# Performance work log

Hardware: AMD Instinct MI355X
Metric: run time of the kernel (lower is better)

The kernel has to match this reference:

```python
import jax, jax.numpy as jnp
import numpy as np

N = 50000
IN_DIM = 128
HEADS = 4
HEAD_DIM = IN_DIM // HEADS
TYPE_NUM = 3
E = 800000
NEG_SLOPE = 0.2


def setup_inputs() -> dict:
    key = jax.random.key(0)
    k1, k2, k3, k4, k5 = jax.random.split(key, 5)
    embedding = jax.random.normal(k1, (N, IN_DIM), dtype=jnp.float32)
    edges = jax.random.randint(k2, (TYPE_NUM, 2, E), 0, N, dtype=jnp.int32)
    W = jax.random.normal(k3, (TYPE_NUM, IN_DIM, HEADS, HEAD_DIM), dtype=jnp.float32) * 0.05
    a_src = jax.random.normal(k4, (TYPE_NUM, HEADS, HEAD_DIM), dtype=jnp.float32) * 0.05
    a_dst = jax.random.normal(k5, (TYPE_NUM, HEADS, HEAD_DIM), dtype=jnp.float32) * 0.05
    return {"embedding": embedding, "edges": edges, "W": W, "a_src": a_src, "a_dst": a_dst}


def _gat_layer(x, ei, W_t, asrc_t, adst_t):
    # x: [N, IN_DIM]; ei: [2, E]; W_t: [IN_DIM, H, D]
    h = jnp.einsum('nd,dhk->nhk', x, W_t)                  # [N, H, D]
    e_src = jnp.sum(h * asrc_t, axis=-1)                   # [N, H]
    e_dst = jnp.sum(h * adst_t, axis=-1)                   # [N, H]
    src, dst = ei[0], ei[1]
    e = jax.nn.leaky_relu(e_src[src] + e_dst[dst], NEG_SLOPE)  # [E, H]
    m = jax.ops.segment_max(e, dst, num_segments=N)        # [N, H]
    e = jnp.exp(e - m[dst])
    denom = jax.ops.segment_sum(e, dst, num_segments=N)    # [N, H]
    msg = h[src] * e[:, :, None]                           # [E, H, D]
    agg = jax.ops.segment_sum(msg, dst, num_segments=N)    # [N, H, D]
    out = agg / (denom[:, :, None] + 1e-9)
    return jax.nn.elu(out.reshape(N, HEADS * HEAD_DIM))


def reference(embedding, edges, W, a_src, a_dst):
    features_gat = [_gat_layer(embedding, edges[i], W[i], a_src[i], a_dst[i])
                    for i in range(TYPE_NUM)]
    # NOTE: the original module (faithfully) also uses the GAT layers for the
    # 'gcn' branch: features_gcn = [self.gat_layers[i](...) for ...]
    features_gcn = [_gat_layer(embedding, edges[i], W[i], a_src[i], a_dst[i])
                    for i in range(TYPE_NUM)]
    return (jnp.stack(features_gat), jnp.stack(features_gcn))
```

## Files before the change

kernel.cpp:

```cpp
#include <hip/hip_runtime.h>
#include <hip/hip_fp16.h>
#include <math.h>

#define NN 50000
#define IND 128
#define NH 4
#define NE 800000
#define NT 3
#define NSLOPE 0.2f

#define TILE 64
#define NBPT 782
#define NBTOT (NT * NBPT)
#define BCAP 1280

#define SCB ((NT * NE + 8191) / 8192)
#define GXB ((NN + 127) / 128)

typedef _Float16 f16x8 __attribute__((ext_vector_type(8)));
typedef float    f32x4 __attribute__((ext_vector_type(4)));

__global__ __launch_bounds__(256) void prep_kernel(
    const float* __restrict__ W, __half* __restrict__ wt16g, int* __restrict__ gcursor)
{
    int idx = blockIdx.x * 256 + threadIdx.x;
    if (idx < NT * IND * IND) {
        int t = idx / (IND * IND), r = idx - t * (IND * IND);
        int k = r >> 7, c = r & 127;
        wt16g[((size_t)t * IND + c) * IND + k] = (__half)W[idx];
    }
    if (idx < NBTOT) gcursor[idx] = idx * BCAP;
}

__global__ __launch_bounds__(512) void scatter_gemm_kernel(
    const int* __restrict__ edges, int* __restrict__ gcursor, unsigned* __restrict__ bucketed,
    const float* __restrict__ x, const __half* __restrict__ wt16g,
    const float* __restrict__ asrc, const float* __restrict__ adst,
    __half* __restrict__ h16, float* __restrict__ es, float* __restrict__ ed)
{
    __shared__ __align__(16) char ldsbuf[34816];
    const int tid = threadIdx.x;

    if (blockIdx.x < SCB) {
        int* cnt = (int*)ldsbuf;
        int* bas = cnt + NBTOT;
        for (int i = tid; i < NBTOT; i += 512) cnt[i] = 0;
        __syncthreads();
        const long long gtot = (long long)NT * NE;
        const long long g0 = (long long)blockIdx.x * 8192;
        long long g1 = g0 + 8192; if (g1 > gtot) g1 = gtot;
        for (long long g = g0 + tid; g < g1; g += 512) {
            int t = (g >= 2LL * NE) ? 2 : (g >= NE ? 1 : 0);
            int e = (int)(g - (long long)t * NE);
            int d = edges[(size_t)t * 2 * NE + NE + e];
            atomicAdd(&cnt[t * NBPT + (d >> 6)], 1);
        }
        __syncthreads();
        for (int i = tid; i < NBTOT; i += 512) {
            int c = cnt[i];
            bas[i] = c ? atomicAdd(&gcursor[i], c) : 0;
            cnt[i] = 0;
        }
        __syncthreads();
        for (long long g = g0 + tid; g < g1; g += 512) {
            int t = (g >= 2LL * NE) ? 2 : (g >= NE ? 1 : 0);
            int e = (int)(g - (long long)t * NE);
            const int* eb = edges + (size_t)t * 2 * NE;
            int s = eb[e], d = eb[NE + e];
            int bg = t * NBPT + (d >> 6);
            int pos = bas[bg] + atomicAdd(&cnt[bg], 1);
            bucketed[pos] = (unsigned)s | ((unsigned)(d & 63) << 16);
        }
        return;
    }

    const int bx = blockIdx.x - SCB;
    const int t  = bx / GXB;
    const int gx = bx - t * GXB;
    __half* tile = (__half*)ldsbuf;
    const int wid = tid >> 6, lane = tid & 63;
    __half* tl = tile + wid * (16 * 136);
    const int l15 = lane & 15, l4 = lane >> 4;
    const int r0 = gx * 128 + wid * 16;
    const bool active = (r0 < NN);

    const __half* wt = wt16g + (size_t)t * IND * IND;
    const float* xrow = x + (size_t)((active ? r0 : 0) + l15) * IND;

    f32x4 acc[8];
    #pragma unroll
    for (int i = 0; i < 8; i++) acc[i] = (f32x4){0.f, 0.f, 0.f, 0.f};

    #pragma unroll
    for (int ks = 0; ks < 4; ks++) {
        const int kb = ks * 32 + l4 * 8;
        float4 x0 = *reinterpret_cast<const float4*>(xrow + kb);
        float4 x1 = *reinterpret_cast<const float4*>(xrow + kb + 4);
        f16x8 af;
        af[0] = (_Float16)x0.x; af[1] = (_Float16)x0.y;
        af[2] = (_Float16)x0.z; af[3] = (_Float16)x0.w;
        af[4] = (_Float16)x1.x; af[5] = (_Float16)x1.y;
        af[6] = (_Float16)x1.z; af[7] = (_Float16)x1.w;
        #pragma unroll
        for (int ct = 0; ct < 8; ct++) {
            f16x8 bf = *reinterpret_cast<const f16x8*>(wt + (size_t)(ct * 16 + l15) * IND + kb);
            acc[ct] = __builtin_amdgcn_mfma_f32_16x16x32_f16(af, bf, acc[ct], 0, 0, 0);
        }
    }

    #pragma unroll
    for (int ct = 0; ct < 8; ct++)
        #pragma unroll
        for (int r = 0; r < 4; r++)
            tl[(l4 * 4 + r) * 136 + ct * 16 + l15] = (__half)acc[ct][r];
    __syncthreads();

    if (active) {
        #pragma unroll
        for (int i = 0; i < 4; i++) {
            int c = lane + 64 * i;
            int row = c >> 4, off = (c & 15) * 8;
            f16x8 v = *reinterpret_cast<const f16x8*>(tl + row * 136 + off);
            *reinterpret_cast<f16x8*>(h16 + ((size_t)t * NN + r0 + row) * IND + off) = v;
        }
        int row16 = lane >> 2, head = lane & 3;
        const __half* hr = tl + row16 * 136 + head * 32;
        const float* av = asrc + ((size_t)t * NH + head) * 32;
        const float* bv = adst + ((size_t)t * NH + head) * 32;
        float se = 0.f, de = 0.f;
        #pragma unroll
        for (int jj = 0; jj < 4; jj++) {
            f16x8 hv = *reinterpret_cast<const f16x8*>(hr + jj * 8);
            #pragma unroll
            for (int j = 0; j < 8; j++) {
                float hf = (float)hv[j];
                se = fmaf(hf, av[jj * 8 + j], se);
                de = fmaf(hf, bv[jj * 8 + j], de);
            }
        }
        int n = r0 + row16;
        es[((size_t)t * NN + n) * NH + head] = se;
        ed[((size_t)t * NN + n) * NH + head] = de;
    }
}

__global__ __launch_bounds__(512) void gat_bucket_kernel(
    const unsigned* __restrict__ bucketed, const int* __restrict__ gcursor,
    const float* __restrict__ es, const float* __restrict__ ed,
    const __half* __restrict__ h16, float* __restrict__ out)
{
    __shared__ unsigned pk[BCAP];
    __shared__ unsigned srt[BCAP];
    __shared__ int hist[TILE], scn[TILE], cur[TILE];
    const int bg = blockIdx.x;
    const int t = bg / NBPT;
    const int node0 = (bg - t * NBPT) * TILE;
    const int tid = threadIdx.x;
    const int base = bg * BCAP;
    const int cnt = gcursor[bg] - base;

    if (tid < TILE) { hist[tid] = 0; cur[tid] = 0; }
    __syncthreads();
    for (int i = tid; i < cnt; i += 512) {
        unsigned v = bucketed[base + i];
        pk[i] = v;
        atomicAdd(&hist[(v >> 16) & 63u], 1);
    }
    __syncthreads();
    if (tid < 64) {
        int v = hist[tid];
        int inc = v;
        #pragma unroll
        for (int off = 1; off < 64; off <<= 1) {
            int n = __shfl_up(inc, off, 64);
            if (tid >= off) inc += n;
        }
        scn[tid] = inc - v;
    }
    __syncthreads();
    for (int i = tid; i < cnt; i += 512) {
        unsigned v = pk[i];
        int dl = (int)((v >> 16) & 63u);
        int pos = scn[dl] + atomicAdd(&cur[dl], 1);
        srt[pos] = v & 0xFFFFu;
    }
    __syncthreads();

    const int wid = tid >> 6, lane = tid & 63;
    const int el = lane >> 5, dl2 = lane & 31;
    const int hsel = dl2 >> 3;
    const float* es_t = es + (size_t)t * NN * NH;
    const __half* h16_t = h16 + (size_t)t * NN * IND;

    for (int j = 0; j < 8; j++) {
        const int dloc = wid * 8 + j;
        const int node = node0 + dloc;
        if (node >= NN) break;
        const int beg = scn[dloc], nE = hist[dloc];
        const float edv = ed[((size_t)t * NN + node) * NH + (lane & 3)];

        float a0 = 0.f, a1 = 0.f, a2 = 0.f, a3 = 0.f, dsum = 0.f;

        for (int b2 = 0; b2 < nE; b2 += 16) {
            int ne = nE - b2; if (ne > 16) ne = 16;
            const int ei = lane >> 2;
            float wv = 0.f; int sv = 0;
            if (ei < ne) {
                sv = (int)srt[beg + b2 + ei];
                float s = es_t[(sv << 2) + (lane & 3)] + edv;
                s = s > 0.f ? s : NSLOPE * s;
                wv = __expf(s);
                dsum += wv;
            }
            int kk = 0;
            for (; kk + 2 <= ne; kk += 2) {
                int k2 = kk + el;
                int   sb = __shfl(sv, k2 << 2, 64);
                float wb = __shfl(wv, (k2 << 2) | hsel, 64);
                uint2 hv = *reinterpret_cast<const uint2*>(h16_t + ((size_t)sb << 7) + (dl2 << 2));
                asm("v_fma_mix_f32 %0, %1, %2, %0 op_sel:[0,0,0] op_sel_hi:[1,0,0]" : "+v"(a0) : "v"(hv.x), "v"(wb));
                asm("v_fma_mix_f32 %0, %1, %2, %0 op_sel:[1,0,0] op_sel_hi:[1,0,0]" : "+v"(a1) : "v"(hv.x), "v"(wb));
                asm("v_fma_mix_f32 %0, %1, %2, %0 op_sel:[0,0,0] op_sel_hi:[1,0,0]" : "+v"(a2) : "v"(hv.y), "v"(wb));
                asm("v_fma_mix_f32 %0, %1, %2, %0 op_sel:[1,0,0] op_sel_hi:[1,0,0]" : "+v"(a3) : "v"(hv.y), "v"(wb));
            }
            if (kk < ne) {
                int   sb = __shfl(sv, kk << 2, 64);
                float wb = __shfl(wv, (kk << 2) | hsel, 64);
                if (el == 0) {
                    uint2 hv = *reinterpret_cast<const uint2*>(h16_t + ((size_t)sb << 7) + (dl2 << 2));
                    asm("v_fma_mix_f32 %0, %1, %2, %0 op_sel:[0,0,0] op_sel_hi:[1,0,0]" : "+v"(a0) : "v"(hv.x), "v"(wb));
                    asm("v_fma_mix_f32 %0, %1, %2, %0 op_sel:[1,0,0] op_sel_hi:[1,0,0]" : "+v"(a1) : "v"(hv.x), "v"(wb));
                    asm("v_fma_mix_f32 %0, %1, %2, %0 op_sel:[0,0,0] op_sel_hi:[1,0,0]" : "+v"(a2) : "v"(hv.y), "v"(wb));
                    asm("v_fma_mix_f32 %0, %1, %2, %0 op_sel:[1,0,0] op_sel_hi:[1,0,0]" : "+v"(a3) : "v"(hv.y), "v"(wb));
                }
            }
        }

        #pragma unroll
        for (int m = 4; m <= 32; m <<= 1) dsum += __shfl_xor(dsum, m, 64);
        a0 += __shfl_xor(a0, 32, 64);
        a1 += __shfl_xor(a1, 32, 64);
        a2 += __shfl_xor(a2, 32, 64);
        a3 += __shfl_xor(a3, 32, 64);
        float dn = __shfl(dsum, hsel, 64) + 1e-9f;

        if (el == 0) {
            float v0 = a0 / dn, v1 = a1 / dn, v2 = a2 / dn, v3 = a3 / dn;
            f32x4 o;
            o[0] = v0 > 0.f ? v0 : expm1f(v0);
            o[1] = v1 > 0.f ? v1 : expm1f(v1);
            o[2] = v2 > 0.f ? v2 : expm1f(v2);
            o[3] = v3 > 0.f ? v3 : expm1f(v3);
            float* obase = out + (size_t)t * NN * IND + ((size_t)node << 7) + (dl2 << 2);
            __builtin_nontemporal_store(o, reinterpret_cast<f32x4*>(obase));
            __builtin_nontemporal_store(o, reinterpret_cast<f32x4*>(obase + (size_t)NT * NN * IND));
        }
    }
}

extern "C" void kernel_launch(void* const* d_in, const int* in_sizes, int n_in,
                              void* d_out, int out_size, void* d_ws, size_t ws_size,
                              hipStream_t stream)
{
    const float* x     = (const float*)d_in[0];
    const int*   edges = (const int*)d_in[1];
    const float* W     = (const float*)d_in[2];
    const float* asrc  = (const float*)d_in[3];
    const float* adst  = (const float*)d_in[4];
    float* out = (float*)d_out;

    char* p = (char*)d_ws;
    __half*   h16      = (__half*)p;   p += (size_t)NT * NN * IND * 2;
    float*    es       = (float*)p;    p += (size_t)NT * NN * NH * 4;
    float*    ed       = (float*)p;    p += (size_t)NT * NN * NH * 4;
    int*      gcursor  = (int*)p;      p += (size_t)NBTOT * 4;
    __half*   wt16g    = (__half*)p;   p += (size_t)NT * IND * IND * 2;
    unsigned* bucketed = (unsigned*)p; p += ((size_t)NBTOT * BCAP + 1024) * 4;

    prep_kernel<<<(NT * IND * IND + 255) / 256, 256, 0, stream>>>(W, wt16g, gcursor);
    scatter_gemm_kernel<<<SCB + NT * GXB, 512, 0, stream>>>(
        edges, gcursor, bucketed, x, wt16g, asrc, adst, h16, es, ed);
    gat_bucket_kernel<<<NBTOT, 512, 0, stream>>>(bucketed, gcursor, es, ed, h16, out);
}
```

Before: 226.5 us.

## Aggregate raw features before projection and fold attention vectors into W

Uses linearity to swap projection and aggregation. Per-head attention logits are computed straight from x through precomputed W·a vectors with a small MFMA. Edges then gather a shared fp16 copy of x instead of per-type projected h. The per-head aggregated features (512 wide per node) then go through a per-type MFMA GEMM with fused ELU and a dual store. This shrinks the gather working set to one fp16 copy of x shared across types, at the cost of 4x-wider gather accumulators, a g16 round trip, and six extra serialized launches.

```diff
diff --git a/kernel.cpp b/kernel.cpp
--- a/kernel.cpp
+++ b/kernel.cpp
@@ -15,13 +15,14 @@
 #define BCAP 1280
 
 #define SCB ((NT * NE + 8191) / 8192)
-#define GXB ((NN + 127) / 128)
+#define CVB ((NN + 127) / 128)
 
 typedef _Float16 f16x8 __attribute__((ext_vector_type(8)));
 typedef float    f32x4 __attribute__((ext_vector_type(4)));
 
 __global__ __launch_bounds__(256) void prep_kernel(
-    const float* __restrict__ W, __half* __restrict__ wt16g, int* __restrict__ gcursor)
+    const float* __restrict__ W, const float* __restrict__ asrc, const float* __restrict__ adst,
+    __half* __restrict__ wt16g, __half* __restrict__ vab16, int* __restrict__ gcursor)
 {
     int idx = blockIdx.x * 256 + threadIdx.x;
     if (idx < NT * IND * IND) {
@@ -29,21 +30,32 @@
         int k = r >> 7, c = r & 127;
         wt16g[((size_t)t * IND + c) * IND + k] = (__half)W[idx];
     }
+    if (idx < 32 * 128) {
+        int c = idx >> 7, d = idx & 127;
+        float acc = 0.f;
+        if (c < 24) {
+            int cc = c < 12 ? c : c - 12;
+            int t = cc >> 2, hd = cc & 3;
+            const float* wrow = W + ((size_t)(t * IND + d) * NH + hd) * 32;
+            const float* av = (c < 12 ? asrc : adst) + ((size_t)t * NH + hd) * 32;
+            #pragma unroll
+            for (int dk = 0; dk < 32; dk++) acc = fmaf(wrow[dk], av[dk], acc);
+        }
+        vab16[idx] = (__half)acc;
+    }
     if (idx < NBTOT) gcursor[idx] = idx * BCAP;
 }
 
-__global__ __launch_bounds__(512) void scatter_gemm_kernel(
+__global__ __launch_bounds__(512) void scatter_conv_kernel(
     const int* __restrict__ edges, int* __restrict__ gcursor, unsigned* __restrict__ bucketed,
-    const float* __restrict__ x, const __half* __restrict__ wt16g,
-    const float* __restrict__ asrc, const float* __restrict__ adst,
-    __half* __restrict__ h16, float* __restrict__ es, float* __restrict__ ed)
-{
-    __shared__ __align__(16) char ldsbuf[34816];
+    const float* __restrict__ x, const __half* __restrict__ vab16,
+    __half* __restrict__ x16, float* __restrict__ es, float* __restrict__ ed)
+{
     const int tid = threadIdx.x;
 
     if (blockIdx.x < SCB) {
-        int* cnt = (int*)ldsbuf;
-        int* bas = cnt + NBTOT;
+        __shared__ int cnt[NBTOT];
+        __shared__ int bas[NBTOT];
         for (int i = tid; i < NBTOT; i += 512) cnt[i] = 0;
         __syncthreads();
         const long long gtot = (long long)NT * NE;
@@ -75,86 +87,58 @@
     }
 
     const int bx = blockIdx.x - SCB;
-    const int t  = bx / GXB;
-    const int gx = bx - t * GXB;
-    __half* tile = (__half*)ldsbuf;
     const int wid = tid >> 6, lane = tid & 63;
-    __half* tl = tile + wid * (16 * 136);
     const int l15 = lane & 15, l4 = lane >> 4;
-    const int r0 = gx * 128 + wid * 16;
-    const bool active = (r0 < NN);
-
-    const __half* wt = wt16g + (size_t)t * IND * IND;
-    const float* xrow = x + (size_t)((active ? r0 : 0) + l15) * IND;
-
-    f32x4 acc[8];
-    #pragma unroll
-    for (int i = 0; i < 8; i++) acc[i] = (f32x4){0.f, 0.f, 0.f, 0.f};
-
+    const int r0 = bx * 128 + wid * 16;
+    if (r0 >= NN) return;
+
+    const float* xrow = x + (size_t)(r0 + l15) * IND;
+    __half* x16row = x16 + (size_t)(r0 + l15) * IND;
+
+    f32x4 acc0 = {0.f,0.f,0.f,0.f}, acc1 = {0.f,0.f,0.f,0.f};
     #pragma unroll
     for (int ks = 0; ks < 4; ks++) {
         const int kb = ks * 32 + l4 * 8;
-        float4 x0 = *reinterpret_cast<const float4*>(xrow + kb);
-        float4 x1 = *reinterpret_cast<const float4*>(xrow + kb + 4);
+        float4 a = *reinterpret_cast<const float4*>(xrow + kb);
+        float4 b = *reinterpret_cast<const float4*>(xrow + kb + 4);
         f16x8 af;
-        af[0] = (_Float16)x0.x; af[1] = (_Float16)x0.y;
-        af[2] = (_Float16)x0.z; af[3] = (_Float16)x0.w;
-        af[4] = (_Float16)x1.x; af[5] = (_Float16)x1.y;
-        af[6] = (_Float16)x1.z; af[7] = (_Float16)x1.w;
-        #pragma unroll
-        for (int ct = 0; ct < 8; ct++) {
-            f16x8 bf = *reinterpret_cast<const f16x8*>(wt + (size_t)(ct * 16 + l15) * IND + kb);
-            acc[ct] = __builtin_amdgcn_mfma_f32_16x16x32_f16(af, bf, acc[ct], 0, 0, 0);
-        }
-    }
-
-    #pragma unroll
-    for (int ct = 0; ct < 8; ct++)
-        #pragma unroll
-        for (int r = 0; r < 4; r++)
-            tl[(l4 * 4 + r) * 136 + ct * 16 + l15] = (__half)acc[ct][r];
-    __syncthreads();
-
-    if (active) {
-        #pragma unroll
-        for (int i = 0; i < 4; i++) {
-            int c = lane + 64 * i;
-            int row = c >> 4, off = (c & 15) * 8;
-            f16x8 v = *reinterpret_cast<const f16x8*>(tl + row * 136 + off);
-            *reinterpret_cast<f16x8*>(h16 + ((size_t)t * NN + r0 + row) * IND + off) = v;
-        }
-        int row16 = lane >> 2, head = lane & 3;
-        const __half* hr = tl + row16 * 136 + head * 32;
-        const float* av = asrc + ((size_t)t * NH + head) * 32;
-        const float* bv = adst + ((size_t)t * NH + head) * 32;
-        float se = 0.f, de = 0.f;
-        #pragma unroll
-        for (int jj = 0; jj < 4; jj++) {
-            f16x8 hv = *reinterpret_cast<const f16x8*>(hr + jj * 8);
-            #pragma unroll
-            for (int j = 0; j < 8; j++) {
-                float hf = (float)hv[j];
-                se = fmaf(hf, av[jj * 8 + j], se);
-                de = fmaf(hf, bv[jj * 8 + j], de);
-            }
-        }
-        int n = r0 + row16;
-        es[((size_t)t * NN + n) * NH + head] = se;
-        ed[((size_t)t * NN + n) * NH + head] = de;
-    }
-}
-
-__global__ __launch_bounds__(512) void gat_bucket_kernel(
+        af[0] = (_Float16)a.x; af[1] = (_Float16)a.y;
+        af[2] = (_Float16)a.z; af[3] = (_Float16)a.w;
+        af[4] = (_Float16)b.x; af[5] = (_Float16)b.y;
+        af[6] = (_Float16)b.z; af[7] = (_Float16)b.w;
+        *reinterpret_cast<f16x8*>(x16row + kb) = af;
+        f16x8 b0 = *reinterpret_cast<const f16x8*>((const __half*)vab16 + (size_t)l15 * IND + kb);
+        f16x8 b1 = *reinterpret_cast<const f16x8*>((const __half*)vab16 + (size_t)(16 + l15) * IND + kb);
+        acc0 = __builtin_amdgcn_mfma_f32_16x16x32_f16(af, b0, acc0, 0, 0, 0);
+        acc1 = __builtin_amdgcn_mfma_f32_16x16x32_f16(af, b1, acc1, 0, 0, 0);
+    }
+    #pragma unroll
+    for (int r = 0; r < 4; r++) {
+        int n = r0 + l4 * 4 + r;
+        float v0 = acc0[r], v1 = acc1[r];
+        if (l15 < 12) {
+            es[((size_t)(l15 >> 2) * NN + n) * NH + (l15 & 3)] = v0;
+        } else {
+            int cc = l15 - 12;
+            ed[((size_t)(cc >> 2) * NN + n) * NH + (cc & 3)] = v0;
+        }
+        if (l15 < 8) {
+            int cc = l15 + 4;
+            ed[((size_t)(cc >> 2) * NN + n) * NH + (cc & 3)] = v1;
+        }
+    }
+}
+
+__global__ __launch_bounds__(512) void gat_gather_kernel(
     const unsigned* __restrict__ bucketed, const int* __restrict__ gcursor,
-    const float* __restrict__ es, const float* __restrict__ ed,
-    const __half* __restrict__ h16, float* __restrict__ out)
+    const float* __restrict__ es_t, const float* __restrict__ ed_t,
+    const __half* __restrict__ x16, __half* __restrict__ g16, int tbase)
 {
     __shared__ unsigned pk[BCAP];
     __shared__ unsigned srt[BCAP];
     __shared__ int hist[TILE], scn[TILE], cur[TILE];
-    const int bg = blockIdx.x;
-    const int t = bg / NBPT;
-    const int node0 = (bg - t * NBPT) * TILE;
+    const int bg = tbase + blockIdx.x;
+    const int node0 = blockIdx.x * TILE;
     const int tid = threadIdx.x;
     const int base = bg * BCAP;
     const int cnt = gcursor[bg] - base;
@@ -187,19 +171,17 @@
     __syncthreads();
 
     const int wid = tid >> 6, lane = tid & 63;
-    const int el = lane >> 5, dl2 = lane & 31;
-    const int hsel = dl2 >> 3;
-    const float* es_t = es + (size_t)t * NN * NH;
-    const __half* h16_t = h16 + (size_t)t * NN * IND;
+    const int hd  = lane >> 4;
+    const int dl3 = lane & 15;
 
     for (int j = 0; j < 8; j++) {
         const int dloc = wid * 8 + j;
         const int node = node0 + dloc;
         if (node >= NN) break;
         const int beg = scn[dloc], nE = hist[dloc];
-        const float edv = ed[((size_t)t * NN + node) * NH + (lane & 3)];
-
-        float a0 = 0.f, a1 = 0.f, a2 = 0.f, a3 = 0.f, dsum = 0.f;
+        const float edv = ed_t[(size_t)node * NH + (lane & 3)];
+
+        float a0=0.f,a1=0.f,a2=0.f,a3=0.f,a4=0.f,a5=0.f,a6=0.f,a7=0.f,dsum=0.f;
 
         for (int b2 = 0; b2 < nE; b2 += 16) {
             int ne = nE - b2; if (ne > 16) ne = 16;
@@ -212,48 +194,75 @@
                 wv = __expf(s);
                 dsum += wv;
             }
-            int kk = 0;
-            for (; kk + 2 <= ne; kk += 2) {
-                int k2 = kk + el;
-                int   sb = __shfl(sv, k2 << 2, 64);
-                float wb = __shfl(wv, (k2 << 2) | hsel, 64);
-                uint2 hv = *reinterpret_cast<const uint2*>(h16_t + ((size_t)sb << 7) + (dl2 << 2));
+            for (int k = 0; k < ne; k++) {
+                int   sb = __shfl(sv, k << 2, 64);
+                float wb = __shfl(wv, (k << 2) | hd, 64);
+                uint4 hv = *reinterpret_cast<const uint4*>(x16 + ((size_t)sb << 7) + (dl3 << 3));
                 asm("v_fma_mix_f32 %0, %1, %2, %0 op_sel:[0,0,0] op_sel_hi:[1,0,0]" : "+v"(a0) : "v"(hv.x), "v"(wb));
                 asm("v_fma_mix_f32 %0, %1, %2, %0 op_sel:[1,0,0] op_sel_hi:[1,0,0]" : "+v"(a1) : "v"(hv.x), "v"(wb));
                 asm("v_fma_mix_f32 %0, %1, %2, %0 op_sel:[0,0,0] op_sel_hi:[1,0,0]" : "+v"(a2) : "v"(hv.y), "v"(wb));
                 asm("v_fma_mix_f32 %0, %1, %2, %0 op_sel:[1,0,0] op_sel_hi:[1,0,0]" : "+v"(a3) : "v"(hv.y), "v"(wb));
-            }
-            if (kk < ne) {
-                int   sb = __shfl(sv, kk << 2, 64);
-                float wb = __shfl(wv, (kk << 2) | hsel, 64);
-                if (el == 0) {
-                    uint2 hv = *reinterpret_cast<const uint2*>(h16_t + ((size_t)sb << 7) + (dl2 << 2));
-                    asm("v_fma_mix_f32 %0, %1, %2, %0 op_sel:[0,0,0] op_sel_hi:[1,0,0]" : "+v"(a0) : "v"(hv.x), "v"(wb));
-                    asm("v_fma_mix_f32 %0, %1, %2, %0 op_sel:[1,0,0] op_sel_hi:[1,0,0]" : "+v"(a1) : "v"(hv.x), "v"(wb));
-                    asm("v_fma_mix_f32 %0, %1, %2, %0 op_sel:[0,0,0] op_sel_hi:[1,0,0]" : "+v"(a2) : "v"(hv.y), "v"(wb));
-                    asm("v_fma_mix_f32 %0, %1, %2, %0 op_sel:[1,0,0] op_sel_hi:[1,0,0]" : "+v"(a3) : "v"(hv.y), "v"(wb));
-                }
+                asm("v_fma_mix_f32 %0, %1, %2, %0 op_sel:[0,0,0] op_sel_hi:[1,0,0]" : "+v"(a4) : "v"(hv.z), "v"(wb));
+                asm("v_fma_mix_f32 %0, %1, %2, %0 op_sel:[1,0,0] op_sel_hi:[1,0,0]" : "+v"(a5) : "v"(hv.z), "v"(wb));
+                asm("v_fma_mix_f32 %0, %1, %2, %0 op_sel:[0,0,0] op_sel_hi:[1,0,0]" : "+v"(a6) : "v"(hv.w), "v"(wb));
+                asm("v_fma_mix_f32 %0, %1, %2, %0 op_sel:[1,0,0] op_sel_hi:[1,0,0]" : "+v"(a7) : "v"(hv.w), "v"(wb));
             }
         }
 
         #pragma unroll
         for (int m = 4; m <= 32; m <<= 1) dsum += __shfl_xor(dsum, m, 64);
-        a0 += __shfl_xor(a0, 32, 64);
-        a1 += __shfl_xor(a1, 32, 64);
-        a2 += __shfl_xor(a2, 32, 64);
-        a3 += __shfl_xor(a3, 32, 64);
-        float dn = __shfl(dsum, hsel, 64) + 1e-9f;
-
-        if (el == 0) {
-            float v0 = a0 / dn, v1 = a1 / dn, v2 = a2 / dn, v3 = a3 / dn;
-            f32x4 o;
-            o[0] = v0 > 0.f ? v0 : expm1f(v0);
-            o[1] = v1 > 0.f ? v1 : expm1f(v1);
-            o[2] = v2 > 0.f ? v2 : expm1f(v2);
-            o[3] = v3 > 0.f ? v3 : expm1f(v3);
-            float* obase = out + (size_t)t * NN * IND + ((size_t)node << 7) + (dl2 << 2);
-            __builtin_nontemporal_store(o, reinterpret_cast<f32x4*>(obase));
-            __builtin_nontemporal_store(o, reinterpret_cast<f32x4*>(obase + (size_t)NT * NN * IND));
+        float rn = 1.f / (__shfl(dsum, hd, 64) + 1e-9f);
+
+        f16x8 g;
+        g[0] = (_Float16)(a0 * rn); g[1] = (_Float16)(a1 * rn);
+        g[2] = (_Float16)(a2 * rn); g[3] = (_Float16)(a3 * rn);
+        g[4] = (_Float16)(a4 * rn); g[5] = (_Float16)(a5 * rn);
+        g[6] = (_Float16)(a6 * rn); g[7] = (_Float16)(a7 * rn);
+        *reinterpret_cast<f16x8*>(g16 + (size_t)node * 512 + lane * 8) = g;
+    }
+}
+
+__global__ __launch_bounds__(256) void out_gemm_kernel(
+    const __half* __restrict__ g16, const __half* __restrict__ wt,
+    float* __restrict__ outa, float* __restrict__ outb)
+{
+    const int tid = threadIdx.x;
+    const int wid = tid >> 6, lane = tid & 63;
+    const int l15 = lane & 15, l4 = lane >> 4;
+    const int n0 = blockIdx.x * 64 + wid * 16;
+    if (n0 >= NN) return;
+
+    const __half* grow = g16 + (size_t)(n0 + l15) * 512;
+
+    f32x4 acc[8];
+    #pragma unroll
+    for (int i = 0; i < 8; i++) acc[i] = (f32x4){0.f,0.f,0.f,0.f};
+
+    #pragma unroll
+    for (int ks = 0; ks < 4; ks++) {
+        const int kb = ks * 32 + l4 * 8;
+        f16x8 af0 = *reinterpret_cast<const f16x8*>(grow + 0 * IND + kb);
+        f16x8 af1 = *reinterpret_cast<const f16x8*>(grow + 1 * IND + kb);
+        f16x8 af2 = *reinterpret_cast<const f16x8*>(grow + 2 * IND + kb);
+        f16x8 af3 = *reinterpret_cast<const f16x8*>(grow + 3 * IND + kb);
+        #pragma unroll
+        for (int ct = 0; ct < 8; ct++) {
+            f16x8 bf = *reinterpret_cast<const f16x8*>(wt + (size_t)(ct * 16 + l15) * IND + kb);
+            f16x8 af = (ct < 2) ? af0 : (ct < 4) ? af1 : (ct < 6) ? af2 : af3;
+            acc[ct] = __builtin_amdgcn_mfma_f32_16x16x32_f16(af, bf, acc[ct], 0, 0, 0);
+        }
+    }
+
+    #pragma unroll
+    for (int ct = 0; ct < 8; ct++) {
+        #pragma unroll
+        for (int r = 0; r < 4; r++) {
+            int n = n0 + l4 * 4 + r;
+            float v = acc[ct][r];
+            float o = v > 0.f ? v : expm1f(v);
+            size_t off = (size_t)n * IND + ct * 16 + l15;
+            __builtin_nontemporal_store(o, outa + off);
+            __builtin_nontemporal_store(o, outb + off);
         }
     }
 }
@@ -270,15 +279,27 @@
     float* out = (float*)d_out;
 
     char* p = (char*)d_ws;
-    __half*   h16      = (__half*)p;   p += (size_t)NT * NN * IND * 2;
+    __half*   x16      = (__half*)p;   p += (size_t)NN * IND * 2;
+    __half*   g16      = (__half*)p;   p += (size_t)NN * 512 * 2;
     float*    es       = (float*)p;    p += (size_t)NT * NN * NH * 4;
     float*    ed       = (float*)p;    p += (size_t)NT * NN * NH * 4;
     int*      gcursor  = (int*)p;      p += (size_t)NBTOT * 4;
     __half*   wt16g    = (__half*)p;   p += (size_t)NT * IND * IND * 2;
+    __half*   vab16    = (__half*)p;   p += (size_t)32 * IND * 2;
     unsigned* bucketed = (unsigned*)p; p += ((size_t)NBTOT * BCAP + 1024) * 4;
 
-    prep_kernel<<<(NT * IND * IND + 255) / 256, 256, 0, stream>>>(W, wt16g, gcursor);
-    scatter_gemm_kernel<<<SCB + NT * GXB, 512, 0, stream>>>(
-        edges, gcursor, bucketed, x, wt16g, asrc, adst, h16, es, ed);
-    gat_bucket_kernel<<<NBTOT, 512, 0, stream>>>(bucketed, gcursor, es, ed, h16, out);
-}
+    prep_kernel<<<(NT * IND * IND + 255) / 256, 256, 0, stream>>>(
+        W, asrc, adst, wt16g, vab16, gcursor);
+    scatter_conv_kernel<<<SCB + CVB, 512, 0, stream>>>(
+        edges, gcursor, bucketed, x, vab16, x16, es, ed);
+
+    for (int t = 0; t < NT; t++) {
+        gat_gather_kernel<<<NBPT, 512, 0, stream>>>(
+            bucketed, gcursor,
+            es + (size_t)t * NN * NH, ed + (size_t)t * NN * NH,
+            x16, g16, t * NBPT);
+        out_gemm_kernel<<<(NN + 63) / 64, 256, 0, stream>>>(
+            g16, wt16g + (size_t)t * IND * IND,
+            out + (size_t)t * NN * IND, out + (size_t)(NT + t) * NN * IND);
+    }
+}
```

New measurement: 367.1 us. +62.1%, slower.

## Split GAT aggregation per edge type and overlap fp16-to-fp32 output expansion

Applied to the files above, without the earlier changes.

The single aggregation kernel is split into one launch per edge type. Each launch writes its result as fp16 to a workspace buffer, and extra blocks in the next launch expand the previous type's fp16 output into the two fp32 output copies. The aim is to shrink the random-access aggregation's store traffic and the cache pollution from the duplicated writes, and to overlap the streaming stores with the next type's gather work. The cost is extra launches, an added fp16 round trip, and fp16 rounding of the final outputs, which changes precision.

```diff
diff --git a/kernel.cpp b/kernel.cpp
--- a/kernel.cpp
+++ b/kernel.cpp
@@ -16,8 +16,10 @@
 
 #define SCB ((NT * NE + 8191) / 8192)
 #define GXB ((NN + 127) / 128)
+#define DUPB 782
 
 typedef _Float16 f16x8 __attribute__((ext_vector_type(8)));
+typedef _Float16 f16x4 __attribute__((ext_vector_type(4)));
 typedef float    f32x4 __attribute__((ext_vector_type(4)));
 
 __global__ __launch_bounds__(256) void prep_kernel(
@@ -82,10 +84,10 @@
     __half* tl = tile + wid * (16 * 136);
     const int l15 = lane & 15, l4 = lane >> 4;
     const int r0 = gx * 128 + wid * 16;
-    const bool active = (r0 < NN);
+    if (r0 >= NN) return;
 
     const __half* wt = wt16g + (size_t)t * IND * IND;
-    const float* xrow = x + (size_t)((active ? r0 : 0) + l15) * IND;
+    const float* xrow = x + (size_t)(r0 + l15) * IND;
 
     f32x4 acc[8];
     #pragma unroll
@@ -115,7 +117,7 @@
             tl[(l4 * 4 + r) * 136 + ct * 16 + l15] = (__half)acc[ct][r];
     __syncthreads();
 
-    if (active) {
+    {
         #pragma unroll
         for (int i = 0; i < 4; i++) {
             int c = lane + 64 * i;
@@ -144,18 +146,45 @@
     }
 }
 
-__global__ __launch_bounds__(512) void gat_bucket_kernel(
+__global__ __launch_bounds__(512) void gat_phase_kernel(
     const unsigned* __restrict__ bucketed, const int* __restrict__ gcursor,
     const float* __restrict__ es, const float* __restrict__ ed,
-    const __half* __restrict__ h16, float* __restrict__ out)
+    const __half* __restrict__ h16, __half* __restrict__ o16,
+    float* __restrict__ out, int tcur, int ngb, int tprev)
 {
     __shared__ unsigned pk[BCAP];
     __shared__ unsigned srt[BCAP];
     __shared__ int hist[TILE], scn[TILE], cur[TILE];
-    const int bg = blockIdx.x;
-    const int t = bg / NBPT;
-    const int node0 = (bg - t * NBPT) * TILE;
     const int tid = threadIdx.x;
+
+    if ((int)blockIdx.x >= ngb) {
+        const size_t tot = (size_t)NN * IND;
+        size_t g0 = (size_t)(blockIdx.x - ngb) * 8192 + (size_t)tid * 16;
+        if (g0 >= tot) return;
+        const __half* src = o16 + (size_t)tprev * tot + g0;
+        float* oa = out + (size_t)tprev * tot + g0;
+        float* ob = oa + (size_t)NT * tot;
+        f16x8 v0 = *reinterpret_cast<const f16x8*>(src);
+        f16x8 v1 = *reinterpret_cast<const f16x8*>(src + 8);
+        f32x4 wq[4];
+        #pragma unroll
+        for (int i = 0; i < 4; i++) wq[0][i] = (float)v0[i];
+        #pragma unroll
+        for (int i = 0; i < 4; i++) wq[1][i] = (float)v0[4 + i];
+        #pragma unroll
+        for (int i = 0; i < 4; i++) wq[2][i] = (float)v1[i];
+        #pragma unroll
+        for (int i = 0; i < 4; i++) wq[3][i] = (float)v1[4 + i];
+        #pragma unroll
+        for (int i = 0; i < 4; i++) {
+            __builtin_nontemporal_store(wq[i], reinterpret_cast<f32x4*>(oa + 4 * i));
+            __builtin_nontemporal_store(wq[i], reinterpret_cast<f32x4*>(ob + 4 * i));
+        }
+        return;
+    }
+
+    const int bg = tcur * NBPT + blockIdx.x;
+    const int node0 = blockIdx.x * TILE;
     const int base = bg * BCAP;
     const int cnt = gcursor[bg] - base;
 
@@ -189,15 +218,15 @@
     const int wid = tid >> 6, lane = tid & 63;
     const int el = lane >> 5, dl2 = lane & 31;
     const int hsel = dl2 >> 3;
-    const float* es_t = es + (size_t)t * NN * NH;
-    const __half* h16_t = h16 + (size_t)t * NN * IND;
+    const float* es_t = es + (size_t)tcur * NN * NH;
+    const __half* h16_t = h16 + (size_t)tcur * NN * IND;
 
     for (int j = 0; j < 8; j++) {
         const int dloc = wid * 8 + j;
         const int node = node0 + dloc;
         if (node >= NN) break;
         const int beg = scn[dloc], nE = hist[dloc];
-        const float edv = ed[((size_t)t * NN + node) * NH + (lane & 3)];
+        const float edv = ed[((size_t)tcur * NN + node) * NH + (lane & 3)];
 
         float a0 = 0.f, a1 = 0.f, a2 = 0.f, a3 = 0.f, dsum = 0.f;
 
@@ -245,15 +274,14 @@
         float dn = __shfl(dsum, hsel, 64) + 1e-9f;
 
         if (el == 0) {
-            float v0 = a0 / dn, v1 = a1 / dn, v2 = a2 / dn, v3 = a3 / dn;
-            f32x4 o;
-            o[0] = v0 > 0.f ? v0 : expm1f(v0);
-            o[1] = v1 > 0.f ? v1 : expm1f(v1);
-            o[2] = v2 > 0.f ? v2 : expm1f(v2);
-            o[3] = v3 > 0.f ? v3 : expm1f(v3);
-            float* obase = out + (size_t)t * NN * IND + ((size_t)node << 7) + (dl2 << 2);
-            __builtin_nontemporal_store(o, reinterpret_cast<f32x4*>(obase));
-            __builtin_nontemporal_store(o, reinterpret_cast<f32x4*>(obase + (size_t)NT * NN * IND));
+            float rn = 1.f / dn;
+            float v0 = a0 * rn, v1 = a1 * rn, v2 = a2 * rn, v3 = a3 * rn;
+            f16x4 o;
+            o[0] = (_Float16)(v0 > 0.f ? v0 : expm1f(v0));
+            o[1] = (_Float16)(v1 > 0.f ? v1 : expm1f(v1));
+            o[2] = (_Float16)(v2 > 0.f ? v2 : expm1f(v2));
+            o[3] = (_Float16)(v3 > 0.f ? v3 : expm1f(v3));
+            *reinterpret_cast<f16x4*>(o16 + ((size_t)tcur * NN + node) * IND + (dl2 << 2)) = o;
         }
     }
 }
@@ -271,6 +299,7 @@
 
     char* p = (char*)d_ws;
     __half*   h16      = (__half*)p;   p += (size_t)NT * NN * IND * 2;
+    __half*   o16      = (__half*)p;   p += (size_t)NT * NN * IND * 2;
     float*    es       = (float*)p;    p += (size_t)NT * NN * NH * 4;
     float*    ed       = (float*)p;    p += (size_t)NT * NN * NH * 4;
     int*      gcursor  = (int*)p;      p += (size_t)NBTOT * 4;
@@ -280,5 +309,13 @@
     prep_kernel<<<(NT * IND * IND + 255) / 256, 256, 0, stream>>>(W, wt16g, gcursor);
     scatter_gemm_kernel<<<SCB + NT * GXB, 512, 0, stream>>>(
         edges, gcursor, bucketed, x, wt16g, asrc, adst, h16, es, ed);
-    gat_bucket_kernel<<<NBTOT, 512, 0, stream>>>(bucketed, gcursor, es, ed, h16, out);
+
+    gat_phase_kernel<<<NBPT, 512, 0, stream>>>(
+        bucketed, gcursor, es, ed, h16, o16, out, 0, NBPT, 0);
+    gat_phase_kernel<<<NBPT + DUPB, 512, 0, stream>>>(
+        bucketed, gcursor, es, ed, h16, o16, out, 1, NBPT, 0);
+    gat_phase_kernel<<<NBPT + DUPB, 512, 0, stream>>>(
+        bucketed, gcursor, es, ed, h16, o16, out, 2, NBPT, 1);
+    gat_phase_kernel<<<DUPB, 512, 0, stream>>>(
+        bucketed, gcursor, es, ed, h16, o16, out, 0, 0, 2);
 }
```

Result: slower. 408.6 us (+80.4%).

## Shrink dst tiles to 48 nodes and gather four edges per wave with 16B loads

Applied to the files above, without the earlier changes.

Destination buckets shrink from 64 to 48 nodes, which yields more gather blocks. Each wave now handles 6 nodes instead of 8. The aggregation loop splits a wave into four 16-lane groups, each processing a different edge with 16-byte row loads, where before two groups used 8-byte loads. A two-step cross-lane reduction combines the groups. The aim is more memory-level parallelism and more blocks in flight for the irregular gather. Smaller changes include nontemporal loads of the bucketed edges, a reciprocal multiply instead of four divides, and an early return for out-of-range waves in the projection kernel. The early return comes before a __syncthreads, so it depends on that barrier tolerating exited waves. The wider per-lane accumulators also raise register use.

```diff
diff --git a/kernel.cpp b/kernel.cpp
--- a/kernel.cpp
+++ b/kernel.cpp
@@ -9,10 +9,10 @@
 #define NT 3
 #define NSLOPE 0.2f
 
-#define TILE 64
-#define NBPT 782
+#define TILE 48
+#define NBPT 1042
 #define NBTOT (NT * NBPT)
-#define BCAP 1280
+#define BCAP 960
 
 #define SCB ((NT * NE + 8191) / 8192)
 #define GXB ((NN + 127) / 128)
@@ -53,7 +53,7 @@
             int t = (g >= 2LL * NE) ? 2 : (g >= NE ? 1 : 0);
             int e = (int)(g - (long long)t * NE);
             int d = edges[(size_t)t * 2 * NE + NE + e];
-            atomicAdd(&cnt[t * NBPT + (d >> 6)], 1);
+            atomicAdd(&cnt[t * NBPT + d / TILE], 1);
         }
         __syncthreads();
         for (int i = tid; i < NBTOT; i += 512) {
@@ -67,9 +67,10 @@
             int e = (int)(g - (long long)t * NE);
             const int* eb = edges + (size_t)t * 2 * NE;
             int s = eb[e], d = eb[NE + e];
-            int bg = t * NBPT + (d >> 6);
+            int bkt = d / TILE;
+            int bg = t * NBPT + bkt;
             int pos = bas[bg] + atomicAdd(&cnt[bg], 1);
-            bucketed[pos] = (unsigned)s | ((unsigned)(d & 63) << 16);
+            bucketed[pos] = (unsigned)s | ((unsigned)(d - bkt * TILE) << 16);
         }
         return;
     }
@@ -82,10 +83,10 @@
     __half* tl = tile + wid * (16 * 136);
     const int l15 = lane & 15, l4 = lane >> 4;
     const int r0 = gx * 128 + wid * 16;
-    const bool active = (r0 < NN);
+    if (r0 >= NN) return;
 
     const __half* wt = wt16g + (size_t)t * IND * IND;
-    const float* xrow = x + (size_t)((active ? r0 : 0) + l15) * IND;
+    const float* xrow = x + (size_t)(r0 + l15) * IND;
 
     f32x4 acc[8];
     #pragma unroll
@@ -115,7 +116,7 @@
             tl[(l4 * 4 + r) * 136 + ct * 16 + l15] = (__half)acc[ct][r];
     __syncthreads();
 
-    if (active) {
+    {
         #pragma unroll
         for (int i = 0; i < 4; i++) {
             int c = lane + 64 * i;
@@ -151,7 +152,7 @@
 {
     __shared__ unsigned pk[BCAP];
     __shared__ unsigned srt[BCAP];
-    __shared__ int hist[TILE], scn[TILE], cur[TILE];
+    __shared__ int hist[64], scn[64], cur[64];
     const int bg = blockIdx.x;
     const int t = bg / NBPT;
     const int node0 = (bg - t * NBPT) * TILE;
@@ -159,10 +160,10 @@
     const int base = bg * BCAP;
     const int cnt = gcursor[bg] - base;
 
-    if (tid < TILE) { hist[tid] = 0; cur[tid] = 0; }
+    if (tid < 64) { hist[tid] = 0; cur[tid] = 0; }
     __syncthreads();
     for (int i = tid; i < cnt; i += 512) {
-        unsigned v = bucketed[base + i];
+        unsigned v = __builtin_nontemporal_load(&bucketed[base + i]);
         pk[i] = v;
         atomicAdd(&hist[(v >> 16) & 63u], 1);
     }
@@ -187,19 +188,20 @@
     __syncthreads();
 
     const int wid = tid >> 6, lane = tid & 63;
-    const int el = lane >> 5, dl2 = lane & 31;
-    const int hsel = dl2 >> 3;
+    const int el2 = lane >> 4;
+    const int dl3 = lane & 15;
+    const int hsel = dl3 >> 2;
     const float* es_t = es + (size_t)t * NN * NH;
     const __half* h16_t = h16 + (size_t)t * NN * IND;
 
-    for (int j = 0; j < 8; j++) {
-        const int dloc = wid * 8 + j;
+    for (int j = 0; j < 6; j++) {
+        const int dloc = wid * 6 + j;
         const int node = node0 + dloc;
         if (node >= NN) break;
         const int beg = scn[dloc], nE = hist[dloc];
         const float edv = ed[((size_t)t * NN + node) * NH + (lane & 3)];
 
-        float a0 = 0.f, a1 = 0.f, a2 = 0.f, a3 = 0.f, dsum = 0.f;
+        float a0=0.f,a1=0.f,a2=0.f,a3=0.f,a4=0.f,a5=0.f,a6=0.f,a7=0.f,dsum=0.f;
 
         for (int b2 = 0; b2 < nE; b2 += 16) {
             int ne = nE - b2; if (ne > 16) ne = 16;
@@ -212,48 +214,54 @@
                 wv = __expf(s);
                 dsum += wv;
             }
-            int kk = 0;
-            for (; kk + 2 <= ne; kk += 2) {
-                int k2 = kk + el;
-                int   sb = __shfl(sv, k2 << 2, 64);
-                float wb = __shfl(wv, (k2 << 2) | hsel, 64);
-                uint2 hv = *reinterpret_cast<const uint2*>(h16_t + ((size_t)sb << 7) + (dl2 << 2));
-                asm("v_fma_mix_f32 %0, %1, %2, %0 op_sel:[0,0,0] op_sel_hi:[1,0,0]" : "+v"(a0) : "v"(hv.x), "v"(wb));
-                asm("v_fma_mix_f32 %0, %1, %2, %0 op_sel:[1,0,0] op_sel_hi:[1,0,0]" : "+v"(a1) : "v"(hv.x), "v"(wb));
-                asm("v_fma_mix_f32 %0, %1, %2, %0 op_sel:[0,0,0] op_sel_hi:[1,0,0]" : "+v"(a2) : "v"(hv.y), "v"(wb));
-                asm("v_fma_mix_f32 %0, %1, %2, %0 op_sel:[1,0,0] op_sel_hi:[1,0,0]" : "+v"(a3) : "v"(hv.y), "v"(wb));
-            }
-            if (kk < ne) {
-                int   sb = __shfl(sv, kk << 2, 64);
-                float wb = __shfl(wv, (kk << 2) | hsel, 64);
-                if (el == 0) {
-                    uint2 hv = *reinterpret_cast<const uint2*>(h16_t + ((size_t)sb << 7) + (dl2 << 2));
+            for (int kk = 0; kk < ne; kk += 4) {
+                int sl = (kk + el2) << 2;
+                int   sb = __shfl(sv, sl, 64);
+                float wb = __shfl(wv, sl | hsel, 64);
+                if (kk + el2 < ne) {
+                    uint4 hv = *reinterpret_cast<const uint4*>(h16_t + ((size_t)sb << 7) + (dl3 << 3));
                     asm("v_fma_mix_f32 %0, %1, %2, %0 op_sel:[0,0,0] op_sel_hi:[1,0,0]" : "+v"(a0) : "v"(hv.x), "v"(wb));
                     asm("v_fma_mix_f32 %0, %1, %2, %0 op_sel:[1,0,0] op_sel_hi:[1,0,0]" : "+v"(a1) : "v"(hv.x), "v"(wb));
                     asm("v_fma_mix_f32 %0, %1, %2, %0 op_sel:[0,0,0] op_sel_hi:[1,0,0]" : "+v"(a2) : "v"(hv.y), "v"(wb));
                     asm("v_fma_mix_f32 %0, %1, %2, %0 op_sel:[1,0,0] op_sel_hi:[1,0,0]" : "+v"(a3) : "v"(hv.y), "v"(wb));
+                    asm("v_fma_mix_f32 %0, %1, %2, %0 op_sel:[0,0,0] op_sel_hi:[1,0,0]" : "+v"(a4) : "v"(hv.z), "v"(wb));
+                    asm("v_fma_mix_f32 %0, %1, %2, %0 op_sel:[1,0,0] op_sel_hi:[1,0,0]" : "+v"(a5) : "v"(hv.z), "v"(wb));
+                    asm("v_fma_mix_f32 %0, %1, %2, %0 op_sel:[0,0,0] op_sel_hi:[1,0,0]" : "+v"(a6) : "v"(hv.w), "v"(wb));
+                    asm("v_fma_mix_f32 %0, %1, %2, %0 op_sel:[1,0,0] op_sel_hi:[1,0,0]" : "+v"(a7) : "v"(hv.w), "v"(wb));
                 }
             }
         }
 
         #pragma unroll
         for (int m = 4; m <= 32; m <<= 1) dsum += __shfl_xor(dsum, m, 64);
-        a0 += __shfl_xor(a0, 32, 64);
-        a1 += __shfl_xor(a1, 32, 64);
-        a2 += __shfl_xor(a2, 32, 64);
-        a3 += __shfl_xor(a3, 32, 64);
+        #pragma unroll
+        for (int m = 16; m <= 32; m <<= 1) {
+            a0 += __shfl_xor(a0, m, 64); a1 += __shfl_xor(a1, m, 64);
+            a2 += __shfl_xor(a2, m, 64); a3 += __shfl_xor(a3, m, 64);
+            a4 += __shfl_xor(a4, m, 64); a5 += __shfl_xor(a5, m, 64);
+            a6 += __shfl_xor(a6, m, 64); a7 += __shfl_xor(a7, m, 64);
+        }
         float dn = __shfl(dsum, hsel, 64) + 1e-9f;
 
-        if (el == 0) {
-            float v0 = a0 / dn, v1 = a1 / dn, v2 = a2 / dn, v3 = a3 / dn;
-            f32x4 o;
-            o[0] = v0 > 0.f ? v0 : expm1f(v0);
-            o[1] = v1 > 0.f ? v1 : expm1f(v1);
-            o[2] = v2 > 0.f ? v2 : expm1f(v2);
-            o[3] = v3 > 0.f ? v3 : expm1f(v3);
-            float* obase = out + (size_t)t * NN * IND + ((size_t)node << 7) + (dl2 << 2);
-            __builtin_nontemporal_store(o, reinterpret_cast<f32x4*>(obase));
-            __builtin_nontemporal_store(o, reinterpret_cast<f32x4*>(obase + (size_t)NT * NN * IND));
+        if (el2 == 0) {
+            float rn = 1.f / dn;
+            float v0=a0*rn, v1=a1*rn, v2=a2*rn, v3=a3*rn;
+            float v4=a4*rn, v5=a5*rn, v6=a6*rn, v7=a7*rn;
+            f32x4 o0, o1;
+            o0[0] = v0 > 0.f ? v0 : expm1f(v0);
+            o0[1] = v1 > 0.f ? v1 : expm1f(v1);
+            o0[2] = v2 > 0.f ? v2 : expm1f(v2);
+            o0[3] = v3 > 0.f ? v3 : expm1f(v3);
+            o1[0] = v4 > 0.f ? v4 : expm1f(v4);
+            o1[1] = v5 > 0.f ? v5 : expm1f(v5);
+            o1[2] = v6 > 0.f ? v6 : expm1f(v6);
+            o1[3] = v7 > 0.f ? v7 : expm1f(v7);
+            float* obase = out + (size_t)t * NN * IND + ((size_t)node << 7) + (dl3 << 3);
+            float* obase2 = obase + (size_t)NT * NN * IND;
+            __builtin_nontemporal_store(o0, reinterpret_cast<f32x4*>(obase));
+            __builtin_nontemporal_store(o1, reinterpret_cast<f32x4*>(obase + 4));
+            __builtin_nontemporal_store(o0, reinterpret_cast<f32x4*>(obase2));
+            __builtin_nontemporal_store(o1, reinterpret_cast<f32x4*>(obase2 + 4));
         }
     }
 }
```

Measured after the change: 203.7 us. -10.0%, faster.
